# Kernel optimization log

Hardware: AMD Instinct MI355X
Metric: run time of the kernel (lower is better)

## Reference

```python
import jax, jax.numpy as jnp
import numpy as np
from jax import lax

RIVER_LENGTH = 50000.0
NUM_SEGMENTS = 20
DT = 3600.0
DX = RIVER_LENGTH / NUM_SEGMENTS
CFL = min(2.0 * DT / DX, 0.9)  # c=2.0 hard-coded in original; clipped to 0.9


def setup_inputs() -> dict:
    key = jax.random.key(0)
    ks = jax.random.split(key, 5)
    B, T = 8192, 4096
    return {
        "runoff": jax.random.uniform(ks[0], (B, T), dtype=jnp.float32) * 10.0,  # mm/hr
        "basin_area": jax.random.uniform(ks[1], (B, 1), dtype=jnp.float32) * 1000.0 + 10.0,  # km^2
        "manning_n": jax.random.uniform(ks[2], (B, 1), dtype=jnp.float32) * 0.05 + 0.01,
        "slope": jax.random.uniform(ks[3], (B, 1), dtype=jnp.float32) * 0.01 + 1e-4,
        "width": jax.random.uniform(ks[4], (B, 1), dtype=jnp.float32) * 50.0 + 1.0,
    }


def reference(runoff, basin_area, manning_n, slope, width):
    # lateral inflow per segment: mm/hr -> m^3/s over basin area, split into segments
    area_m2 = basin_area * 1e6  # (B,1)
    q_lateral = runoff / 1000.0 / 3600.0 * area_m2 / float(NUM_SEGMENTS)  # (B,T)

    B = runoff.shape[0]
    Q0 = jnp.zeros((B, NUM_SEGMENTS + 1), dtype=runoff.dtype)

    def step(Q, q_in):
        # upwind update for segments 1..N using OLD state (matches tf version)
        q_in = q_in[:, None]  # (B,1)
        Q_upd = jnp.maximum(Q[:, 1:] - CFL * (Q[:, 1:] - Q[:, :-1]) + q_in * DT, 0.0)
        Q_new = jnp.concatenate([Q[:, :1], Q_upd], axis=1)  # segment 0 unchanged (stays 0)
        return Q_new, Q_new[:, -1]

    _, outlet = lax.scan(step, Q0, q_lateral.T)  # outlet: (T,B)
    return outlet.T  # (B,T) discharge in m^3/s
```

## Files before the change

### kernel.cpp

```cpp
#include <hip/hip_runtime.h>


#define KTAPS 32
#define RPT   8
#define TPB   256
#define TILE_T (TPB * RPT)
#define NQ   ((TILE_T + KTAPS) / 4)

struct WTab { float w[KTAPS]; };

__device__ __forceinline__ int swz(int q) { return q ^ ((q >> 3) & 7); }

__global__ __launch_bounds__(TPB) void kwr_fir_lds_kernel(
    const float* __restrict__ runoff,
    const float* __restrict__ basin_area,
    float* __restrict__ out,
    int T, int tiles_per_row, WTab wt)
{
    __shared__ float4 lds[NQ];

    const int tid  = threadIdx.x;
    const int blk  = blockIdx.x;
    const int b    = blk / tiles_per_row;
    const int tile = blk - b * tiles_per_row;
    const long long rowbase = (long long)b * T;
    const int tstart = tile * TILE_T - KTAPS;

    const float4* gsrc = (const float4*)(runoff + rowbase + tstart);
    #pragma unroll
    for (int pass = 0; pass < 3; ++pass) {
        int q = tid + pass * TPB;
        if (q < NQ) {
            float4 v;
            if (tstart + 4 * q >= 0) v = gsrc[q];
            else                     v = make_float4(0.f, 0.f, 0.f, 0.f);
            lds[swz(q)] = v;
        }
    }
    __syncthreads();

    float buf[RPT + KTAPS];
    #pragma unroll
    for (int c = 0; c < (RPT + KTAPS) / 4; ++c) {
        float4 v = lds[swz(2 * tid + c)];
        buf[4*c+0] = v.x; buf[4*c+1] = v.y;
        buf[4*c+2] = v.z; buf[4*c+3] = v.w;
    }

    float acc[RPT];
    {
        float S = 0.0f;
        #pragma unroll
        for (int m = 13; m <= 32; ++m) S += buf[m];
        acc[0] = S;
        #pragma unroll
        for (int r = 1; r < RPT; ++r) {
            S += buf[r + 32] - buf[r + 12];
            acc[r] = S;
        }
    }
    #pragma unroll
    for (int k = 20; k < KTAPS; ++k) {
        const float wk = wt.w[k];
        #pragma unroll
        for (int r = 0; r < RPT; ++r)
            acc[r] = fmaf(wk, buf[32 + r - k], acc[r]);
    }

    const float s = basin_area[b] * 50.0f;
    float* orow = out + rowbase + tile * TILE_T + tid * RPT;
    ((float4*)orow)[0] = make_float4(acc[0]*s, acc[1]*s, acc[2]*s, acc[3]*s);
    ((float4*)orow)[1] = make_float4(acc[4]*s, acc[5]*s, acc[6]*s, acc[7]*s);
}

extern "C" void kernel_launch(void* const* d_in, const int* in_sizes, int n_in,
                              void* d_out, int out_size, void* d_ws, size_t ws_size,
                              hipStream_t stream)
{
    const float* runoff     = (const float*)d_in[0];
    const float* basin_area = (const float*)d_in[1];
    float* out = (float*)d_out;

    const int B = in_sizes[1];
    const int T = in_sizes[0] / B;

    WTab wt;
    double Q[21];
    for (int j = 0; j <= 20; ++j) Q[j] = (j >= 1) ? 1.0 : 0.0;
    wt.w[0] = 1.0f;
    for (int k = 1; k < KTAPS; ++k) {
        for (int j = 20; j >= 1; --j) Q[j] = 0.1 * Q[j] + 0.9 * Q[j - 1];
        wt.w[k] = (float)Q[20];
    }

    const int tiles_per_row = T / TILE_T;
    const int nblk = B * tiles_per_row;

    kwr_fir_lds_kernel<<<nblk, TPB, 0, stream>>>(runoff, basin_area, out,
                                                 T, tiles_per_row, wt);
}
```

Measured before the change: 233.8 us.

## Convert FIR kernel to persistent blocks with double-buffered LDS prefetch

Replaces one block per tile with a fixed grid of 4096 persistent blocks that loop over tiles. Each block loads the next tile's input into registers while it computes the current tile, then writes it into the alternate LDS buffer. The aim is to hide global load latency behind compute and cut block launch overhead. In exchange it uses twice the LDS and more registers, which may lower occupancy on a kernel that is mostly memory-bound.

```diff
diff --git a/kernel.cpp b/kernel.cpp
--- a/kernel.cpp
+++ b/kernel.cpp
@@ -6,6 +6,7 @@
 #define TPB   256
 #define TILE_T (TPB * RPT)
 #define NQ   ((TILE_T + KTAPS) / 4)
+#define NBLK 4096
 
 struct WTab { float w[KTAPS]; };
 
@@ -15,62 +16,102 @@
     const float* __restrict__ runoff,
     const float* __restrict__ basin_area,
     float* __restrict__ out,
-    int T, int tiles_per_row, WTab wt)
+    int T, int tiles_per_row, int n_tiles, WTab wt)
 {
-    __shared__ float4 lds[NQ];
+    __shared__ float4 lds[2][NQ];
+    const int tid = threadIdx.x;
 
-    const int tid  = threadIdx.x;
-    const int blk  = blockIdx.x;
-    const int b    = blk / tiles_per_row;
-    const int tile = blk - b * tiles_per_row;
-    const long long rowbase = (long long)b * T;
-    const int tstart = tile * TILE_T - KTAPS;
+    float4 st[3];
+    int cur = 0;
+    int ti = blockIdx.x;
 
-    const float4* gsrc = (const float4*)(runoff + rowbase + tstart);
-    #pragma unroll
-    for (int pass = 0; pass < 3; ++pass) {
-        int q = tid + pass * TPB;
-        if (q < NQ) {
-            float4 v;
-            if (tstart + 4 * q >= 0) v = gsrc[q];
-            else                     v = make_float4(0.f, 0.f, 0.f, 0.f);
-            lds[swz(q)] = v;
+    {
+        const int b      = ti / tiles_per_row;
+        const int tile   = ti - b * tiles_per_row;
+        const int tstart = tile * TILE_T - KTAPS;
+        const float4* gsrc = (const float4*)(runoff + (long long)b * T + tstart);
+        #pragma unroll
+        for (int p = 0; p < 3; ++p) {
+            int q = tid + p * TPB;
+            if (q < NQ)
+                st[p] = (tstart + 4 * q >= 0) ? gsrc[q]
+                                              : make_float4(0.f, 0.f, 0.f, 0.f);
+        }
+        #pragma unroll
+        for (int p = 0; p < 3; ++p) {
+            int q = tid + p * TPB;
+            if (q < NQ) lds[0][swz(q)] = st[p];
         }
     }
-    __syncthreads();
 
-    float buf[RPT + KTAPS];
-    #pragma unroll
-    for (int c = 0; c < (RPT + KTAPS) / 4; ++c) {
-        float4 v = lds[swz(2 * tid + c)];
-        buf[4*c+0] = v.x; buf[4*c+1] = v.y;
-        buf[4*c+2] = v.z; buf[4*c+3] = v.w;
+    for (; ti < n_tiles; ti += NBLK) {
+        const int nx = ti + NBLK;
+        __syncthreads();
+
+        if (nx < n_tiles) {
+            const int nb      = nx / tiles_per_row;
+            const int ntile   = nx - nb * tiles_per_row;
+            const int ntstart = ntile * TILE_T - KTAPS;
+            const float4* gsrc =
+                (const float4*)(runoff + (long long)nb * T + ntstart);
+            #pragma unroll
+            for (int p = 0; p < 3; ++p) {
+                int q = tid + p * TPB;
+                if (q < NQ)
+                    st[p] = (ntstart + 4 * q >= 0)
+                                ? gsrc[q] : make_float4(0.f, 0.f, 0.f, 0.f);
+            }
+        }
+
+        {
+            const int b    = ti / tiles_per_row;
+            const int tile = ti - b * tiles_per_row;
+
+            float buf[RPT + KTAPS];
+            #pragma unroll
+            for (int c = 0; c < (RPT + KTAPS) / 4; ++c) {
+                float4 v = lds[cur][swz(2 * tid + c)];
+                buf[4*c+0] = v.x; buf[4*c+1] = v.y;
+                buf[4*c+2] = v.z; buf[4*c+3] = v.w;
+            }
+
+            float acc[RPT];
+            {
+                float S = 0.0f;
+                #pragma unroll
+                for (int m = 13; m <= 32; ++m) S += buf[m];
+                acc[0] = S;
+                #pragma unroll
+                for (int r = 1; r < RPT; ++r) {
+                    S += buf[r + 32] - buf[r + 12];
+                    acc[r] = S;
+                }
+            }
+            #pragma unroll
+            for (int k = 20; k < KTAPS; ++k) {
+                const float wk = wt.w[k];
+                #pragma unroll
+                for (int r = 0; r < RPT; ++r)
+                    acc[r] = fmaf(wk, buf[32 + r - k], acc[r]);
+            }
+
+            const float s = basin_area[b] * 50.0f;
+            float* orow = out + (long long)b * T + tile * TILE_T + tid * RPT;
+            ((float4*)orow)[0] =
+                make_float4(acc[0]*s, acc[1]*s, acc[2]*s, acc[3]*s);
+            ((float4*)orow)[1] =
+                make_float4(acc[4]*s, acc[5]*s, acc[6]*s, acc[7]*s);
+        }
+
+        if (nx < n_tiles) {
+            #pragma unroll
+            for (int p = 0; p < 3; ++p) {
+                int q = tid + p * TPB;
+                if (q < NQ) lds[cur ^ 1][swz(q)] = st[p];
+            }
+        }
+        cur ^= 1;
     }
-
-    float acc[RPT];
-    {
-        float S = 0.0f;
-        #pragma unroll
-        for (int m = 13; m <= 32; ++m) S += buf[m];
-        acc[0] = S;
-        #pragma unroll
-        for (int r = 1; r < RPT; ++r) {
-            S += buf[r + 32] - buf[r + 12];
-            acc[r] = S;
-        }
-    }
-    #pragma unroll
-    for (int k = 20; k < KTAPS; ++k) {
-        const float wk = wt.w[k];
-        #pragma unroll
-        for (int r = 0; r < RPT; ++r)
-            acc[r] = fmaf(wk, buf[32 + r - k], acc[r]);
-    }
-
-    const float s = basin_area[b] * 50.0f;
-    float* orow = out + rowbase + tile * TILE_T + tid * RPT;
-    ((float4*)orow)[0] = make_float4(acc[0]*s, acc[1]*s, acc[2]*s, acc[3]*s);
-    ((float4*)orow)[1] = make_float4(acc[4]*s, acc[5]*s, acc[6]*s, acc[7]*s);
 }
 
 extern "C" void kernel_launch(void* const* d_in, const int* in_sizes, int n_in,
@@ -94,8 +135,9 @@
     }
 
     const int tiles_per_row = T / TILE_T;
-    const int nblk = B * tiles_per_row;
+    const int n_tiles = B * tiles_per_row;
+    const int nblk = (n_tiles < NBLK) ? n_tiles : NBLK;
 
     kwr_fir_lds_kernel<<<nblk, TPB, 0, stream>>>(runoff, basin_area, out,
-                                                 T, tiles_per_row, wt);
+                                                 T, tiles_per_row, n_tiles, wt);
 }
```

Result: no change. 238.0 us (+1.8%).
